# Performance work log

Hardware: AMD Instinct MI355X
Metric: run time of the kernel (lower is better)

The kernel has to match this reference:

```python
import jax, jax.numpy as jnp
import numpy as np

B, N, D_POINTS, D_MODEL = 8, 2048, 64, 512


def _linear_params(key, d_in, d_out, bias=True):
    k1, k2 = jax.random.split(key)
    bound = 1.0 / np.sqrt(d_in)
    W = jax.random.uniform(k1, (d_in, d_out), jnp.float32, -bound, bound)
    if not bias:
        return W
    b = jax.random.uniform(k2, (d_out,), jnp.float32, -bound, bound)
    return W, b


def setup_inputs() -> dict:
    key = jax.random.key(0)
    ks = jax.random.split(key, 10)
    xyz = jax.random.normal(ks[0], (B, N, 3), jnp.float32)
    features = jax.random.normal(ks[1], (B, N, D_POINTS), jnp.float32)
    W1, b1 = _linear_params(ks[2], D_POINTS, D_MODEL)      # fc1
    W2, b2 = _linear_params(ks[3], D_MODEL, D_POINTS)      # fc2
    Wd1, bd1 = _linear_params(ks[4], 3, D_MODEL)           # fc_delta[0]
    Wd2, bd2 = _linear_params(ks[5], D_MODEL, D_MODEL)     # fc_delta[2]
    Wq = _linear_params(ks[6], D_MODEL, D_MODEL, bias=False)
    Wk = _linear_params(ks[7], D_MODEL, D_MODEL, bias=False)
    Wv = _linear_params(ks[8], D_MODEL, D_MODEL, bias=False)
    return {"xyz": xyz, "features": features,
            "W1": W1, "b1": b1, "W2": W2, "b2": b2,
            "Wd1": Wd1, "bd1": bd1, "Wd2": Wd2, "bd2": bd2,
            "Wq": Wq, "Wk": Wk, "Wv": Wv, "k": 16}


def _forward(xyz, features, W1, b1, W2, b2, Wd1, bd1, Wd2, bd2, Wq, Wk, Wv, k):
    # square_distance: ||xi - xj||^2, [B, N, N]
    sq = jnp.sum(xyz * xyz, axis=-1)
    dists = sq[:, :, None] + sq[:, None, :] - 2.0 * jnp.einsum('bnd,bmd->bnm', xyz, xyz)
    knn_idx = jnp.argsort(dists, axis=-1)[:, :, :k]              # [B, N, k]
    knn_xyz = jax.vmap(lambda p, i: p[i])(xyz, knn_idx)          # [B, N, k, 3]

    pre = features
    x = features @ W1 + b1                                       # [B, N, d_model]
    q, key, v = x @ Wq, x @ Wk, x @ Wv

    # fc_delta on gathered neighbor coordinates -> [B, N, k, d_model]
    pos_enc = jax.nn.relu(knn_xyz @ Wd1 + bd1) @ Wd2 + bd2

    eps = 1e-06
    knn_d = jnp.take_along_axis(dists, knn_idx, axis=2)          # [B, N, k]
    weights = 1.0 / (knn_d + eps)
    weighted_avg = jnp.sum(pos_enc * weights[..., None], axis=2) / \
        jnp.sum(weights, axis=2, keepdims=True)                  # [B, N, d_model]

    scale = 1.0 / np.sqrt(D_MODEL)
    score = jnp.einsum('bnd,bmd->bnm', q + weighted_avg, key + weighted_avg) * scale
    attn_map = jax.nn.softmax(score, axis=-1)                    # [B, N, N]
    attn = jnp.einsum('bnm,bmd->bnd', attn_map, v + weighted_avg)
    res = attn @ W2 + b2 + pre                                   # [B, N, d_points]
    return res, attn


def reference(xyz, features, W1, b1, W2, b2, Wd1, bd1, Wd2, bd2, Wq, Wk, Wv, k):
    return _forward(xyz, features, W1, b1, W2, b2, Wd1, bd1, Wd2, bd2, Wq, Wk, Wv, k)
```

## Files before the change

kernel.cpp:

```cpp
#include <hip/hip_runtime.h>

#define BB 8
#define NN 2048
#define DP 64
#define DM 512
#define KNNK 16
#define ROWS (BB*NN)

#define SWZ_SK8(t) (((((t)&3) ^ (((t)>>3)&3)))*8)

typedef __attribute__((ext_vector_type(8))) short s16x8;
typedef __attribute__((ext_vector_type(4))) short s16x4;
typedef __attribute__((ext_vector_type(4))) float f32x4;

__device__ __forceinline__ float bf2f(short u){
  union { unsigned int i; float f; } v; v.i = ((unsigned int)(unsigned short)u) << 16; return v.f;
}
__device__ __forceinline__ short f2bf(float f){
  union { float f; unsigned int i; } v; v.f = f;
  unsigned int x = v.i;
  return (short)((x + 0x7fffu + ((x >> 16) & 1u)) >> 16);
}

__device__ __forceinline__ void gload16(const void* g, void* l){
  __builtin_amdgcn_global_load_lds(
      (const __attribute__((address_space(1))) void*)(__UINTPTR_TYPE__)g,
      (__attribute__((address_space(3))) void*)(__UINTPTR_TYPE__)l, 16, 0, 0);
}

__device__ __forceinline__ unsigned wave_min_u32(unsigned v){
  v = min(v, (unsigned)__builtin_amdgcn_update_dpp((int)v, (int)v, 0x111, 0xF, 0xF, false));
  v = min(v, (unsigned)__builtin_amdgcn_update_dpp((int)v, (int)v, 0x112, 0xF, 0xF, false));
  v = min(v, (unsigned)__builtin_amdgcn_update_dpp((int)v, (int)v, 0x114, 0xF, 0xF, false));
  v = min(v, (unsigned)__builtin_amdgcn_update_dpp((int)v, (int)v, 0x118, 0xF, 0xF, false));
  v = min(v, (unsigned)__builtin_amdgcn_update_dpp((int)v, (int)v, 0x142, 0xF, 0xF, false));
  v = min(v, (unsigned)__builtin_amdgcn_update_dpp((int)v, (int)v, 0x143, 0xF, 0xF, false));
  return (unsigned)__builtin_amdgcn_readlane((int)v, 63);
}

__global__ void k_sq(const float* __restrict__ xyz, float* __restrict__ sq){
  int i = blockIdx.x*256 + threadIdx.x;
  if (i < ROWS){
    float x = xyz[3*i], y = xyz[3*i+1], z = xyz[3*i+2];
    sq[i] = x*x + y*y + z*z;
  }
}

__global__ __launch_bounds__(256) void k_knn(const float* __restrict__ xyz, const float* __restrict__ sq,
        int* __restrict__ kidx, float* __restrict__ kw, float* __restrict__ wsum){
  int row = blockIdx.x*4 + (threadIdx.x >> 6);
  int l = threadIdx.x & 63;
  int b = row >> 11; int i = row & (NN-1);
  const float* xb = xyz + (size_t)b*NN*3;
  const float* sqb = sq + (size_t)b*NN;
  float xi0 = xb[3*i], xi1 = xb[3*i+1], xi2 = xb[3*i+2];
  float sqi = sqb[i];
  unsigned key[32];
  unsigned m1 = 0xFFFFFFFFu, m2 = 0xFFFFFFFFu, m3 = 0xFFFFFFFFu;
  #pragma unroll
  for (int e = 0; e < 32; ++e){
    int j = e*64 + l;
    float d = sqi + sqb[j] - 2.0f*(xi0*xb[3*j] + xi1*xb[3*j+1] + xi2*xb[3*j+2]);
    d = fmaxf(d, 0.f);
    union { float f; unsigned u; } cv; cv.f = d;
    unsigned k = (cv.u & 0xFFFFF800u) | (unsigned)j;
    key[e] = k;
    unsigned r1 = max(k, m1);  m1 = min(k, m1);
    unsigned r2 = max(r1, m2); m2 = min(r1, m2);
    m3 = min(r2, m3);
  }
  float wacc = 0.f;
  for (int sel = 0; sel < KNNK; ++sel){
    unsigned g = wave_min_u32(m1);
    unsigned j = g & 2047u;
    union { unsigned u; float f; } dv; dv.u = g & 0xFFFFF800u;
    float wg = 1.0f/(dv.f + 1e-6f);
    wacc += wg;
    if (l == 0){
      kidx[(size_t)row*KNNK + sel] = (int)j;
      kw[(size_t)row*KNNK + sel] = wg;
    }
    bool win = (m1 == g);
    if (win){ m1 = m2; m2 = m3; m3 = 0xFFFFFFFFu; }
    if (__any(win && m1 == 0xFFFFFFFFu)){
      if (win && m1 == 0xFFFFFFFFu){
        unsigned mm = 0xFFFFFFFFu;
        #pragma unroll
        for (int e = 0; e < 32; ++e){
          unsigned k2 = key[e];
          mm = min(mm, (k2 > g) ? k2 : 0xFFFFFFFFu);
        }
        m1 = mm;
      }
    }
  }
  if (l == 0) wsum[row] = wacc;
}

__global__ void k_prep2(const float* __restrict__ Wq, const float* __restrict__ Wk,
                        const float* __restrict__ Wv, const float* __restrict__ Wd2,
                        const float* __restrict__ W1, const float* __restrict__ W2,
                        const float* __restrict__ feat,
                        short* __restrict__ Wqt, short* __restrict__ Wkt,
                        short* __restrict__ Wvt, short* __restrict__ Wd2t,
                        short* __restrict__ W1t, short* __restrict__ W2t,
                        short* __restrict__ featb){
  int idx = blockIdx.x*256 + threadIdx.x;
  if (idx < 4*DM*DM){
    int m = idx >> 18;
    int r = idx & (DM*DM-1);
    int n = r >> 9, k = r & 511;
    const float* W = (m==0)?Wq:(m==1)?Wk:(m==2)?Wv:Wd2;
    short* Wt = (m==0)?Wqt:(m==1)?Wkt:(m==2)?Wvt:Wd2t;
    Wt[r] = f2bf(W[k*DM + n]);
  } else if (idx < 4*DM*DM + DM*DP){
    int r = idx - 4*DM*DM;
    int n = r >> 6, k = r & 63;
    W1t[r] = f2bf(W1[(size_t)k*DM + n]);
  } else if (idx < 4*DM*DM + 2*DM*DP){
    int r = idx - 4*DM*DM - DM*DP;
    int n = r >> 9, k = r & 511;
    W2t[r] = f2bf(W2[(size_t)k*DP + n]);
  } else {
    int r = idx - 4*DM*DM - 2*DM*DP;
    featb[r] = f2bf(feat[r]);
  }
}

__global__ __launch_bounds__(256) void k_g(const float* __restrict__ xyz, const float* __restrict__ Wd1,
                   const float* __restrict__ bd1, const int* __restrict__ kidx,
                   const float* __restrict__ kw, const float* __restrict__ wsum, short* __restrict__ g){
  int bid = blockIdx.x;
  int p = ((bid&7)<<11) + ((bid>>3)<<2) + (threadIdx.x>>6);
  int c8 = (threadIdx.x&63)*8;
  int b = p >> 11;
  const float* xbase = xyz + (size_t)b*NN*3;
  float wd0[8], wd1v[8], wd2v[8], bb[8];
  #pragma unroll
  for (int e=0;e<8;++e){
    wd0[e]  = Wd1[c8+e];
    wd1v[e] = Wd1[DM + c8+e];
    wd2v[e] = Wd1[2*DM + c8+e];
    bb[e]   = bd1[c8+e];
  }
  int jj[KNNK]; float wj[KNNK];
  #pragma unroll
  for (int j = 0; j < KNNK; ++j){
    jj[j] = kidx[(size_t)p*KNNK + j];
    wj[j] = kw[(size_t)p*KNNK + j];
  }
  float acc[8] = {0,0,0,0,0,0,0,0};
  #pragma unroll
  for (int j = 0; j < KNNK; ++j){
    float x0 = xbase[3*jj[j]], x1 = xbase[3*jj[j]+1], x2 = xbase[3*jj[j]+2];
    float w = wj[j];
    #pragma unroll
    for (int e=0;e<8;++e){
      float v = fmaf(x0, wd0[e], fmaf(x1, wd1v[e], fmaf(x2, wd2v[e], bb[e])));
      acc[e] = fmaf(w, fmaxf(v, 0.f), acc[e]);
    }
  }
  float inv = 1.0f/wsum[p];
  s16x8 o;
  #pragma unroll
  for (int e=0;e<8;++e) o[e] = f2bf(acc[e]*inv);
  *(s16x8*)&g[(size_t)p*DM + c8] = o;
}

template<int KD, int MODE>
__global__ __launch_bounds__(256) void k_gemm(const short* __restrict__ A, const short* __restrict__ Bt,
       const float* __restrict__ bias, const short* __restrict__ addb, short* __restrict__ outb){
  __shared__ short As[128*32];
  __shared__ short Bs[128*32];
  int t = threadIdx.x;
  size_t i0 = (size_t)blockIdx.x*128, n0 = (size_t)blockIdx.y*128;
  int w = t >> 6, l = t & 63, la = l & 15, lg = l >> 4;
  int wr = w >> 1, wc = w & 1;
  int rch8 = (lg ^ ((la>>1)&3))*8;
  f32x4 acc[4][4];
  #pragma unroll
  for (int h=0;h<4;++h)
    #pragma unroll
    for (int c=0;c<4;++c) acc[h][c] = (f32x4){0.f,0.f,0.f,0.f};
  int srow = t >> 2; int sk8 = SWZ_SK8(t);
  const short* Ab  = A  + (i0 + srow)*KD + sk8;
  const short* Ab2 = A  + (i0 + 64 + srow)*KD + sk8;
  const short* Bb  = Bt + (n0 + srow)*KD + sk8;
  const short* Bb2 = Bt + (n0 + 64 + srow)*KD + sk8;
  short* Asd  = &As[t*8];      short* Asd2 = &As[2048 + t*8];
  short* Bsd  = &Bs[t*8];      short* Bsd2 = &Bs[2048 + t*8];
  for (int k0 = 0; k0 < KD; k0 += 32){
    gload16(Ab  + k0, Asd);
    gload16(Ab2 + k0, Asd2);
    gload16(Bb  + k0, Bsd);
    gload16(Bb2 + k0, Bsd2);
    __syncthreads();
    s16x8 af[4], bg[4];
    #pragma unroll
    for (int h=0;h<4;++h) af[h] = *(const s16x8*)&As[(wr*64 + h*16 + la)*32 + rch8];
    #pragma unroll
    for (int c=0;c<4;++c) bg[c] = *(const s16x8*)&Bs[(wc*64 + c*16 + la)*32 + rch8];
    #pragma unroll
    for (int h=0;h<4;++h)
      #pragma unroll
      for (int c=0;c<4;++c)
        acc[h][c] = __builtin_amdgcn_mfma_f32_16x16x32_bf16(af[h], bg[c], acc[h][c], 0, 0, 0);
    __syncthreads();
  }
  #pragma unroll
  for (int h=0;h<4;++h){
    #pragma unroll
    for (int c=0;c<4;++c){
      size_t col = n0 + wc*64 + c*16 + la;
      #pragma unroll
      for (int r=0;r<4;++r){
        size_t row = i0 + wr*64 + h*16 + lg*4 + r;
        float v = acc[h][c][r];
        if (MODE == 0) outb[row*DM + col] = f2bf(v + bias[col]);
        else           outb[row*DM + col] = f2bf(v + bf2f(addb[row*DM + col]));
      }
    }
  }
}

__global__ __launch_bounds__(256) void k_gemm3(const short* __restrict__ A, const short* __restrict__ Bt,
       const short* __restrict__ addb, short* __restrict__ q, short* __restrict__ k, short* __restrict__ v){
  __shared__ short As[128*32];
  __shared__ short Bs[128*32];
  int t = threadIdx.x;
  int by = blockIdx.y;
  short* outb = (by < 4) ? q : (by < 8) ? k : v;
  size_t i0 = (size_t)blockIdx.x*128;
  size_t n0 = (size_t)by*128;
  size_t c0 = (size_t)(by & 3)*128;
  int w = t >> 6, l = t & 63, la = l & 15, lg = l >> 4;
  int wr = w >> 1, wc = w & 1;
  int rch8 = (lg ^ ((la>>1)&3))*8;
  f32x4 acc[4][4];
  #pragma unroll
  for (int h=0;h<4;++h)
    #pragma unroll
    for (int c=0;c<4;++c) acc[h][c] = (f32x4){0.f,0.f,0.f,0.f};
  int srow = t >> 2; int sk8 = SWZ_SK8(t);
  const short* Ab  = A  + (i0 + srow)*DM + sk8;
  const short* Ab2 = A  + (i0 + 64 + srow)*DM + sk8;
  const short* Bb  = Bt + (n0 + srow)*DM + sk8;
  const short* Bb2 = Bt + (n0 + 64 + srow)*DM + sk8;
  short* Asd  = &As[t*8];      short* Asd2 = &As[2048 + t*8];
  short* Bsd  = &Bs[t*8];      short* Bsd2 = &Bs[2048 + t*8];
  for (int k0 = 0; k0 < DM; k0 += 32){
    gload16(Ab  + k0, Asd);
    gload16(Ab2 + k0, Asd2);
    gload16(Bb  + k0, Bsd);
    gload16(Bb2 + k0, Bsd2);
    __syncthreads();
    s16x8 af[4], bg[4];
    #pragma unroll
    for (int h=0;h<4;++h) af[h] = *(const s16x8*)&As[(wr*64 + h*16 + la)*32 + rch8];
    #pragma unroll
    for (int c=0;c<4;++c) bg[c] = *(const s16x8*)&Bs[(wc*64 + c*16 + la)*32 + rch8];
    #pragma unroll
    for (int h=0;h<4;++h)
      #pragma unroll
      for (int c=0;c<4;++c)
        acc[h][c] = __builtin_amdgcn_mfma_f32_16x16x32_bf16(af[h], bg[c], acc[h][c], 0, 0, 0);
    __syncthreads();
  }
  #pragma unroll
  for (int h=0;h<4;++h){
    #pragma unroll
    for (int c=0;c<4;++c){
      size_t col = c0 + wc*64 + c*16 + la;
      #pragma unroll
      for (int r=0;r<4;++r){
        size_t row = i0 + wr*64 + h*16 + lg*4 + r;
        outb[row*DM + col] = f2bf(acc[h][c][r] + bf2f(addb[row*DM + col]));
      }
    }
  }
}

__global__ __launch_bounds__(256) void k_vt(const short* __restrict__ ve, short* __restrict__ vt){
  int j0 = blockIdx.x*32, d0 = blockIdx.y*32, b = blockIdx.z;
  __shared__ short tile[32][36];
  int t = threadIdx.x;
  int r = t >> 3, c4 = (t & 7)*4;
  const short* vb = ve + (size_t)b*NN*DM;
  *(s16x4*)&tile[r][c4] = *(const s16x4*)&vb[(size_t)(j0+r)*DM + d0 + c4];
  __syncthreads();
  s16x4 o;
  #pragma unroll
  for (int e=0;e<4;++e) o[e] = tile[c4+e][r];
  short* ob = vt + (size_t)b*DM*NN;
  *(s16x4*)&ob[(size_t)(d0+r)*NN + j0 + c4] = o;
}

__global__ __launch_bounds__(256) void k_sexp(const short* __restrict__ qe, const short* __restrict__ ke,
       short* __restrict__ pbuf, float* __restrict__ lsum_part){
  __shared__ short As[128*64];
  __shared__ short Bs[128*64];
  int bid = blockIdx.x;
  int b = bid & 7;
  int r2 = bid >> 3;
  int ti = r2 & 15, tj = r2 >> 4;
  size_t i0 = (size_t)ti*128;
  size_t j0 = (size_t)tj*128;
  const short* A  = qe + (size_t)b*NN*DM;
  const short* Bt = ke + (size_t)b*NN*DM;
  int t = threadIdx.x;
  int w = t >> 6, l = t & 63, la = l & 15, lg = l >> 4;
  int wr = w >> 1, wc = w & 1;
  int rs8_0 = ((lg     ) ^ (la&7))*8;
  int rs8_1 = ((lg + 4 ) ^ (la&7))*8;
  f32x4 acc[4][4];
  #pragma unroll
  for (int h=0;h<4;++h)
    #pragma unroll
    for (int c=0;c<4;++c) acc[h][c] = (f32x4){0.f,0.f,0.f,0.f};
  int srow0 = t >> 3;
  int gch8  = (((t&7) ^ ((t>>3)&7)))*8;
  const short* Abase = A  + (i0 + srow0)*DM + gch8;
  const short* Bbase = Bt + (j0 + srow0)*DM + gch8;
  for (int k0 = 0; k0 < DM; k0 += 64){
    #pragma unroll
    for (int q = 0; q < 4; ++q){
      gload16(Abase + (size_t)(q*32)*DM + k0, &As[(q*256 + t)*8]);
      gload16(Bbase + (size_t)(q*32)*DM + k0, &Bs[(q*256 + t)*8]);
    }
    __syncthreads();
    #pragma unroll
    for (int s = 0; s < 2; ++s){
      int rs8 = s ? rs8_1 : rs8_0;
      s16x8 af[4], bg[4];
      #pragma unroll
      for (int h=0;h<4;++h) af[h] = *(const s16x8*)&As[(wr*64 + h*16 + la)*64 + rs8];
      #pragma unroll
      for (int c=0;c<4;++c) bg[c] = *(const s16x8*)&Bs[(wc*64 + c*16 + la)*64 + rs8];
      #pragma unroll
      for (int h=0;h<4;++h)
        #pragma unroll
        for (int c=0;c<4;++c)
          acc[h][c] = __builtin_amdgcn_mfma_f32_16x16x32_bf16(af[h], bg[c], acc[h][c], 0, 0, 0);
    }
    __syncthreads();
  }
  const float scale = 0.044194173824159216f;
  short* pb = pbuf + (size_t)b*NN*NN;
  float rsum[4][4];
  #pragma unroll
  for (int h=0;h<4;++h)
    #pragma unroll
    for (int r=0;r<4;++r) rsum[h][r] = 0.f;
  #pragma unroll
  for (int h=0;h<4;++h){
    #pragma unroll
    for (int c=0;c<4;++c){
      size_t col = j0 + wc*64 + c*16 + la;
      #pragma unroll
      for (int r=0;r<4;++r){
        size_t row = i0 + wr*64 + h*16 + lg*4 + r;
        float p = __expf(acc[h][c][r]*scale);
        rsum[h][r] += p;
        pb[row*NN + col] = f2bf(p);
      }
    }
  }
  #pragma unroll
  for (int m = 1; m < 16; m <<= 1){
    #pragma unroll
    for (int h=0;h<4;++h)
      #pragma unroll
      for (int r=0;r<4;++r) rsum[h][r] += __shfl_xor(rsum[h][r], m);
  }
  if (la == 0){
    float* lp = lsum_part + (size_t)(tj*2 + wc)*ROWS + (size_t)b*NN;
    #pragma unroll
    for (int h=0;h<4;++h)
      #pragma unroll
      for (int r=0;r<4;++r)
        lp[i0 + wr*64 + h*16 + lg*4 + r] = rsum[h][r];
  }
}

__global__ void k_lsum(const float* __restrict__ lsum_part, float* __restrict__ linv){
  int g = blockIdx.x*256 + threadIdx.x;
  float s = 0.f;
  #pragma unroll
  for (int i = 0; i < 32; ++i) s += lsum_part[(size_t)i*ROWS + g];
  linv[g] = 1.0f/s;
}

__global__ __launch_bounds__(512) void k_pv(const short* __restrict__ pbuf, const short* __restrict__ vt,
        const float* __restrict__ linv, float* __restrict__ attn){
  __shared__ short As[128*64];
  __shared__ short Bs[128*64];
  int bid = blockIdx.x;
  int b = bid & 7;
  int r2 = bid >> 3;
  int ti = r2 & 15, tn = r2 >> 4;
  size_t i0 = (size_t)ti*128;
  size_t n0 = (size_t)tn*128;
  const short* A  = pbuf + (size_t)b*NN*NN;
  const short* Bt = vt + (size_t)b*DM*NN;
  int t = threadIdx.x;
  int w = t >> 6, l = t & 63, la = l & 15, lg = l >> 4;
  int wr = w >> 1, wc = w & 1;
  int rs8_0 = ((lg     ) ^ (la&7))*8;
  int rs8_1 = ((lg + 4 ) ^ (la&7))*8;
  f32x4 acc[2][4];
  #pragma unroll
  for (int h=0;h<2;++h)
    #pragma unroll
    for (int c=0;c<4;++c) acc[h][c] = (f32x4){0.f,0.f,0.f,0.f};
  int srow0 = t >> 3;
  int gch8  = (((t&7) ^ ((t>>3)&7)))*8;
  const short* Abase = A  + (i0 + srow0)*NN + gch8;
  const short* Bbase = Bt + (n0 + srow0)*NN + gch8;
  for (int k0 = 0; k0 < NN; k0 += 64){
    #pragma unroll
    for (int q = 0; q < 2; ++q){
      gload16(Abase + (size_t)(q*64)*NN + k0, &As[(q*512 + t)*8]);
      gload16(Bbase + (size_t)(q*64)*NN + k0, &Bs[(q*512 + t)*8]);
    }
    __syncthreads();
    #pragma unroll
    for (int s = 0; s < 2; ++s){
      int rs8 = s ? rs8_1 : rs8_0;
      s16x8 af[2], bg[4];
      #pragma unroll
      for (int h=0;h<2;++h) af[h] = *(const s16x8*)&As[(wr*32 + h*16 + la)*64 + rs8];
      #pragma unroll
      for (int c=0;c<4;++c) bg[c] = *(const s16x8*)&Bs[(wc*64 + c*16 + la)*64 + rs8];
      #pragma unroll
      for (int h=0;h<2;++h)
        #pragma unroll
        for (int c=0;c<4;++c)
          acc[h][c] = __builtin_amdgcn_mfma_f32_16x16x32_bf16(af[h], bg[c], acc[h][c], 0, 0, 0);
    }
    __syncthreads();
  }
  #pragma unroll
  for (int h=0;h<2;++h){
    #pragma unroll
    for (int c=0;c<4;++c){
      size_t col = n0 + wc*64 + c*16 + la;
      #pragma unroll
      for (int r=0;r<4;++r){
        size_t row = i0 + wr*32 + h*16 + lg*4 + r;
        attn[(size_t)b*NN*DM + row*DM + col] = acc[h][c][r] * linv[(size_t)b*NN + row];
      }
    }
  }
}

__global__ __launch_bounds__(256) void k_res(const float* __restrict__ attn, const short* __restrict__ W2t,
       const float* __restrict__ b2, const float* __restrict__ feat, float* __restrict__ res){
  __shared__ short As[64*32];
  __shared__ short Bs[64*32];
  int t = threadIdx.x;
  size_t i0 = (size_t)blockIdx.x*64;
  int w = t >> 6, l = t & 63, la = l & 15, lg = l >> 4;
  int rch8 = (lg ^ ((la>>1)&3))*8;
  f32x4 acc[4];
  #pragma unroll
  for (int c=0;c<4;++c) acc[c] = (f32x4){0.f,0.f,0.f,0.f};
  int srow = t >> 2;
  int ch = t & 3;
  int dsw8 = (ch ^ ((srow>>1)&3))*8;
  int sk8 = SWZ_SK8(t);
  const float* Arow = attn + (i0 + srow)*DM + ch*8;
  for (int k0 = 0; k0 < DM; k0 += 32){
    f32x4 a0 = *(const f32x4*)&Arow[k0];
    f32x4 a1 = *(const f32x4*)&Arow[k0 + 4];
    s16x8 ab;
    #pragma unroll
    for (int e=0;e<4;++e){ ab[e] = f2bf(a0[e]); ab[4+e] = f2bf(a1[e]); }
    *(s16x8*)&As[srow*32 + dsw8] = ab;
    gload16(W2t + (size_t)srow*DM + k0 + sk8, &Bs[t*8]);
    __syncthreads();
    s16x8 af, bg[4];
    af = *(const s16x8*)&As[(w*16 + la)*32 + rch8];
    #pragma unroll
    for (int c=0;c<4;++c) bg[c] = *(const s16x8*)&Bs[(c*16 + la)*32 + rch8];
    #pragma unroll
    for (int c=0;c<4;++c)
      acc[c] = __builtin_amdgcn_mfma_f32_16x16x32_bf16(af, bg[c], acc[c], 0, 0, 0);
    __syncthreads();
  }
  #pragma unroll
  for (int c=0;c<4;++c){
    int col = c*16 + la;
    #pragma unroll
    for (int r=0;r<4;++r){
      size_t row = i0 + w*16 + lg*4 + r;
      res[row*DP + col] = acc[c][r] + b2[col] + feat[row*DP + col];
    }
  }
}

extern "C" void kernel_launch(void* const* d_in, const int* in_sizes, int n_in,
                              void* d_out, int out_size, void* d_ws, size_t ws_size,
                              hipStream_t stream){
  const float* xyz  = (const float*)d_in[0];
  const float* feat = (const float*)d_in[1];
  const float* W1   = (const float*)d_in[2];
  const float* b1   = (const float*)d_in[3];
  const float* W2   = (const float*)d_in[4];
  const float* b2   = (const float*)d_in[5];
  const float* Wd1  = (const float*)d_in[6];
  const float* bd1  = (const float*)d_in[7];
  const float* Wd2  = (const float*)d_in[8];
  const float* bd2  = (const float*)d_in[9];
  const float* Wq   = (const float*)d_in[10];
  const float* Wk   = (const float*)d_in[11];
  const float* Wv   = (const float*)d_in[12];

  char* ws = (char*)d_ws;
  float* sq        = (float*)(ws + (0ull<<20));
  int*   kidx      = (int*)  (ws + (1ull<<20));
  float* kw        = (float*)(ws + (2ull<<20));
  float* wsum      = (float*)(ws + (3ull<<20));
  float* lsum_part = (float*)(ws + (1ull<<20));
  float* linv      = (float*)(ws + (3ull<<20));
  short* Wqt   = (short*)(ws + (4ull<<20));
  short* Wkt   = Wqt + (size_t)DM*DM;
  short* Wvt   = Wkt + (size_t)DM*DM;
  short* Wd2t  = Wvt + (size_t)DM*DM;
  short* W1t   = (short*)(ws + (6ull<<20));
  short* W2t   = (short*)(ws + (6ull<<20) + 131072);
  short* featb = (short*)(ws + (7ull<<20));
  short* qe    = (short*)(ws + (9ull<<20));
  short* g     = (short*)(ws + (25ull<<20));
  short* x     = (short*)(ws + (41ull<<20));
  short* wab   = (short*)(ws + (57ull<<20));
  short* ve    = (short*)(ws + (73ull<<20));
  short* pbuf  = (short*)(ws + (89ull<<20));
  short* ke = g; short* vt = x;

  float* res  = (float*)d_out;
  float* attn = (float*)d_out + (size_t)ROWS*DP;

  k_sq   <<<ROWS/256, 256, 0, stream>>>(xyz, sq);
  k_knn  <<<ROWS/4, 256, 0, stream>>>(xyz, sq, kidx, kw, wsum);
  k_prep2<<<(4*DM*DM + 2*DM*DP + ROWS*DP)/256, 256, 0, stream>>>(
           Wq, Wk, Wv, Wd2, W1, W2, feat, Wqt, Wkt, Wvt, Wd2t, W1t, W2t, featb);
  k_g    <<<ROWS/4, 256, 0, stream>>>(xyz, Wd1, bd1, kidx, kw, wsum, g);
  k_gemm<DP,0>  <<<dim3(ROWS/128, DM/128), 256, 0, stream>>>(featb, W1t, b1, nullptr, x);
  k_gemm<DM,0>  <<<dim3(ROWS/128, DM/128), 256, 0, stream>>>(g, Wd2t, bd2, nullptr, wab);
  k_gemm3       <<<dim3(ROWS/128, 12), 256, 0, stream>>>(x, Wqt, wab, qe, ke, ve);
  k_vt   <<<dim3(NN/32, DM/32, BB), 256, 0, stream>>>(ve, vt);
  k_sexp <<<2048, 256, 0, stream>>>(qe, ke, pbuf, lsum_part);
  k_lsum <<<ROWS/256, 256, 0, stream>>>(lsum_part, linv);
  k_pv   <<<512, 512, 0, stream>>>(pbuf, vt, linv, attn);
  k_res  <<<ROWS/64, 256, 0, stream>>>(attn, W2t, b2, feat, res);
}
```

Before: 251.8 us.

## Fuse sq into knn, fold lsum into pv, widen qkv GEMM tile

Drops the separate squared-norm kernel by recomputing norms inline in the kNN kernel. Folds the softmax row-sum reduction into the PV kernel's prologue, with the inverse sums kept in LDS. Widens the QKV GEMM to 128x256 tiles with 512 threads so fewer blocks each reuse the A tile across more columns. Also swaps the manual bf16 rounding for the HIP intrinsic. Together these remove two launches and some global round trips, at the cost of redundant lsum reads per PV block and recomputed norms.

```diff
diff --git a/kernel.cpp b/kernel.cpp
--- a/kernel.cpp
+++ b/kernel.cpp
@@ -1,4 +1,5 @@
 #include <hip/hip_runtime.h>
+#include <hip/hip_bf16.h>
 
 #define BB 8
 #define NN 2048
@@ -17,9 +18,8 @@
   union { unsigned int i; float f; } v; v.i = ((unsigned int)(unsigned short)u) << 16; return v.f;
 }
 __device__ __forceinline__ short f2bf(float f){
-  union { float f; unsigned int i; } v; v.f = f;
-  unsigned int x = v.i;
-  return (short)((x + 0x7fffu + ((x >> 16) & 1u)) >> 16);
+  __hip_bfloat16 h = __float2bfloat16(f);
+  return *reinterpret_cast<short*>(&h);
 }
 
 __device__ __forceinline__ void gload16(const void* g, void* l){
@@ -38,29 +38,22 @@
   return (unsigned)__builtin_amdgcn_readlane((int)v, 63);
 }
 
-__global__ void k_sq(const float* __restrict__ xyz, float* __restrict__ sq){
-  int i = blockIdx.x*256 + threadIdx.x;
-  if (i < ROWS){
-    float x = xyz[3*i], y = xyz[3*i+1], z = xyz[3*i+2];
-    sq[i] = x*x + y*y + z*z;
-  }
-}
-
-__global__ __launch_bounds__(256) void k_knn(const float* __restrict__ xyz, const float* __restrict__ sq,
+__global__ __launch_bounds__(256) void k_knn(const float* __restrict__ xyz,
         int* __restrict__ kidx, float* __restrict__ kw, float* __restrict__ wsum){
   int row = blockIdx.x*4 + (threadIdx.x >> 6);
   int l = threadIdx.x & 63;
   int b = row >> 11; int i = row & (NN-1);
   const float* xb = xyz + (size_t)b*NN*3;
-  const float* sqb = sq + (size_t)b*NN;
   float xi0 = xb[3*i], xi1 = xb[3*i+1], xi2 = xb[3*i+2];
-  float sqi = sqb[i];
+  float sqi = xi0*xi0 + xi1*xi1 + xi2*xi2;
   unsigned key[32];
   unsigned m1 = 0xFFFFFFFFu, m2 = 0xFFFFFFFFu, m3 = 0xFFFFFFFFu;
   #pragma unroll
   for (int e = 0; e < 32; ++e){
     int j = e*64 + l;
-    float d = sqi + sqb[j] - 2.0f*(xi0*xb[3*j] + xi1*xb[3*j+1] + xi2*xb[3*j+2]);
+    float x0 = xb[3*j], x1 = xb[3*j+1], x2 = xb[3*j+2];
+    float sqj = x0*x0 + x1*x1 + x2*x2;
+    float d = sqi + sqj - 2.0f*(xi0*x0 + xi1*x1 + xi2*x2);
     d = fmaxf(d, 0.f);
     union { float f; unsigned u; } cv; cv.f = d;
     unsigned k = (cv.u & 0xFFFFF800u) | (unsigned)j;
@@ -223,18 +216,18 @@
   }
 }
 
-__global__ __launch_bounds__(256) void k_gemm3(const short* __restrict__ A, const short* __restrict__ Bt,
+__global__ __launch_bounds__(512) void k_gemm3(const short* __restrict__ A, const short* __restrict__ Bt,
        const short* __restrict__ addb, short* __restrict__ q, short* __restrict__ k, short* __restrict__ v){
   __shared__ short As[128*32];
-  __shared__ short Bs[128*32];
+  __shared__ short Bs[256*32];
   int t = threadIdx.x;
   int by = blockIdx.y;
-  short* outb = (by < 4) ? q : (by < 8) ? k : v;
+  short* outb = (by < 2) ? q : (by < 4) ? k : v;
   size_t i0 = (size_t)blockIdx.x*128;
-  size_t n0 = (size_t)by*128;
-  size_t c0 = (size_t)(by & 3)*128;
+  size_t n0 = (size_t)by*256;
+  size_t c0 = (size_t)(by & 1)*256;
   int w = t >> 6, l = t & 63, la = l & 15, lg = l >> 4;
-  int wr = w >> 1, wc = w & 1;
+  int wr = w >> 2, wc = w & 3;
   int rch8 = (lg ^ ((la>>1)&3))*8;
   f32x4 acc[4][4];
   #pragma unroll
@@ -243,14 +236,12 @@
     for (int c=0;c<4;++c) acc[h][c] = (f32x4){0.f,0.f,0.f,0.f};
   int srow = t >> 2; int sk8 = SWZ_SK8(t);
   const short* Ab  = A  + (i0 + srow)*DM + sk8;
-  const short* Ab2 = A  + (i0 + 64 + srow)*DM + sk8;
   const short* Bb  = Bt + (n0 + srow)*DM + sk8;
-  const short* Bb2 = Bt + (n0 + 64 + srow)*DM + sk8;
-  short* Asd  = &As[t*8];      short* Asd2 = &As[2048 + t*8];
-  short* Bsd  = &Bs[t*8];      short* Bsd2 = &Bs[2048 + t*8];
+  const short* Bb2 = Bt + (n0 + 128 + srow)*DM + sk8;
+  short* Asd = &As[t*8];
+  short* Bsd = &Bs[t*8];  short* Bsd2 = &Bs[4096 + t*8];
   for (int k0 = 0; k0 < DM; k0 += 32){
     gload16(Ab  + k0, Asd);
-    gload16(Ab2 + k0, Asd2);
     gload16(Bb  + k0, Bsd);
     gload16(Bb2 + k0, Bsd2);
     __syncthreads();
@@ -382,18 +373,11 @@
   }
 }
 
-__global__ void k_lsum(const float* __restrict__ lsum_part, float* __restrict__ linv){
-  int g = blockIdx.x*256 + threadIdx.x;
-  float s = 0.f;
-  #pragma unroll
-  for (int i = 0; i < 32; ++i) s += lsum_part[(size_t)i*ROWS + g];
-  linv[g] = 1.0f/s;
-}
-
 __global__ __launch_bounds__(512) void k_pv(const short* __restrict__ pbuf, const short* __restrict__ vt,
-        const float* __restrict__ linv, float* __restrict__ attn){
+        const float* __restrict__ lsum_part, float* __restrict__ attn){
   __shared__ short As[128*64];
   __shared__ short Bs[128*64];
+  __shared__ float linv_lds[128];
   int bid = blockIdx.x;
   int b = bid & 7;
   int r2 = bid >> 3;
@@ -407,6 +391,13 @@
   int wr = w >> 1, wc = w & 1;
   int rs8_0 = ((lg     ) ^ (la&7))*8;
   int rs8_1 = ((lg + 4 ) ^ (la&7))*8;
+  if (t < 128){
+    const float* lp = lsum_part + (size_t)b*NN + i0 + t;
+    float s = 0.f;
+    #pragma unroll
+    for (int i = 0; i < 32; ++i) s += lp[(size_t)i*ROWS];
+    linv_lds[t] = 1.0f/s;
+  }
   f32x4 acc[2][4];
   #pragma unroll
   for (int h=0;h<2;++h)
@@ -446,8 +437,8 @@
       size_t col = n0 + wc*64 + c*16 + la;
       #pragma unroll
       for (int r=0;r<4;++r){
-        size_t row = i0 + wr*32 + h*16 + lg*4 + r;
-        attn[(size_t)b*NN*DM + row*DM + col] = acc[h][c][r] * linv[(size_t)b*NN + row];
+        int rl = wr*32 + h*16 + lg*4 + r;
+        attn[(size_t)b*NN*DM + (i0 + rl)*DM + col] = acc[h][c][r] * linv_lds[rl];
       }
     }
   }
@@ -516,12 +507,10 @@
   const float* Wv   = (const float*)d_in[12];
 
   char* ws = (char*)d_ws;
-  float* sq        = (float*)(ws + (0ull<<20));
   int*   kidx      = (int*)  (ws + (1ull<<20));
   float* kw        = (float*)(ws + (2ull<<20));
   float* wsum      = (float*)(ws + (3ull<<20));
   float* lsum_part = (float*)(ws + (1ull<<20));
-  float* linv      = (float*)(ws + (3ull<<20));
   short* Wqt   = (short*)(ws + (4ull<<20));
   short* Wkt   = Wqt + (size_t)DM*DM;
   short* Wvt   = Wkt + (size_t)DM*DM;
@@ -540,17 +529,15 @@
   float* res  = (float*)d_out;
   float* attn = (float*)d_out + (size_t)ROWS*DP;
 
-  k_sq   <<<ROWS/256, 256, 0, stream>>>(xyz, sq);
-  k_knn  <<<ROWS/4, 256, 0, stream>>>(xyz, sq, kidx, kw, wsum);
+  k_knn  <<<ROWS/4, 256, 0, stream>>>(xyz, kidx, kw, wsum);
   k_prep2<<<(4*DM*DM + 2*DM*DP + ROWS*DP)/256, 256, 0, stream>>>(
            Wq, Wk, Wv, Wd2, W1, W2, feat, Wqt, Wkt, Wvt, Wd2t, W1t, W2t, featb);
   k_g    <<<ROWS/4, 256, 0, stream>>>(xyz, Wd1, bd1, kidx, kw, wsum, g);
   k_gemm<DP,0>  <<<dim3(ROWS/128, DM/128), 256, 0, stream>>>(featb, W1t, b1, nullptr, x);
   k_gemm<DM,0>  <<<dim3(ROWS/128, DM/128), 256, 0, stream>>>(g, Wd2t, bd2, nullptr, wab);
-  k_gemm3       <<<dim3(ROWS/128, 12), 256, 0, stream>>>(x, Wqt, wab, qe, ke, ve);
+  k_gemm3       <<<dim3(ROWS/128, 6), 512, 0, stream>>>(x, Wqt, wab, qe, ke, ve);
   k_vt   <<<dim3(NN/32, DM/32, BB), 256, 0, stream>>>(ve, vt);
   k_sexp <<<2048, 256, 0, stream>>>(qe, ke, pbuf, lsum_part);
-  k_lsum <<<ROWS/256, 256, 0, stream>>>(lsum_part, linv);
-  k_pv   <<<512, 512, 0, stream>>>(pbuf, vt, linv, attn);
+  k_pv   <<<512, 512, 0, stream>>>(pbuf, vt, lsum_part, attn);
   k_res  <<<ROWS/64, 256, 0, stream>>>(attn, W2t, b2, feat, res);
 }
```

After: 246.1 us, median of 2. 1.02x faster.
